# Kernel tuning notes

Measured on AMD Instinct MI355X. Metric: run time of the kernel, lower is better.

Reference implementation:

```python
import jax, jax.numpy as jnp
import numpy as np

N = 262144        # tokens routed
D = 1024          # input_dim
E = 64            # num_experts
TOP_K = 2
NOISE_EPS = 1e-05
ALPHA = 10.0


def setup_inputs() -> dict:
    key = jax.random.key(0)
    k1, k2, k3, k4, k5 = jax.random.split(key, 5)
    x = jax.random.normal(k1, (N, D), dtype=jnp.float32)
    # nn.Linear init scale ~ 1/sqrt(fan_in); keep logits at sane magnitude
    gate_w = jax.random.normal(k2, (E, D), dtype=jnp.float32) * (1.0 / np.sqrt(D))
    gate_b = jax.random.normal(k3, (E,), dtype=jnp.float32) * 0.01
    # w_noise is initialized to zeros in the module; use small random values
    # so the noise path is exercised
    w_noise = jax.random.normal(k4, (E, E), dtype=jnp.float32) * 0.01
    noise = jax.random.normal(k5, (N, E), dtype=jnp.float32)  # torch.randn_like
    return {"x": x, "gate_w": gate_w, "gate_b": gate_b,
            "w_noise": w_noise, "noise": noise}


def reference(x, gate_w, gate_b, w_noise, noise):
    # gate linear: [N, D] @ [D, E] + [E]
    clean_logits = jnp.einsum('nd,ed->ne', x, gate_w) + gate_b
    # training-mode learnable noise injection
    raw_noise_stddev = clean_logits @ w_noise                 # [N, E]
    noise_stddev = jax.nn.softplus(raw_noise_stddev) + NOISE_EPS
    logits = clean_logits + noise * noise_stddev              # noisy_logits

    # decompostion_tp: k-th largest per row (kthvalue(n - k + 1) == k-th largest)
    kth_largest = jax.lax.top_k(logits, TOP_K)[0][:, -1]       # [N]
    mask = logits < kth_largest[:, None]                       # strictly below kth
    sm = jax.nn.softmax(logits, axis=1)
    out = jnp.where(mask,
                    ALPHA * jnp.log1p(sm),      # alpha * log(sm + 1)
                    ALPHA * jnp.expm1(sm))      # alpha * (exp(sm) - 1)

    gates = jax.nn.softmax(out, axis=1)
    return gates
```

## Files before the change

### kernel.cpp

```cpp
#include <hip/hip_runtime.h>

typedef _Float16 half8v __attribute__((ext_vector_type(8)));
typedef float f32x4 __attribute__((ext_vector_type(4)));

constexpr float INV4096 = 1.0f / 4096.0f;
constexpr float ALPHA = 10.0f;

__device__ __forceinline__ f32x4 mfma16(half8v a, half8v b, f32x4 c_) {
  return __builtin_amdgcn_mfma_f32_16x16x32_f16(a, b, c_, 0, 0, 0);
}
__device__ __forceinline__ void dma16(const void *g, void *l) {
  __builtin_amdgcn_global_load_lds(
      (const __attribute__((address_space(1))) void *)g,
      (__attribute__((address_space(3))) void *)l, 16, 0, 0);
}
template <int N> __device__ __forceinline__ void wait_vm() {
  asm volatile("s_waitcnt vmcnt(%0)" ::"n"(N) : "memory");
}

__global__ __launch_bounds__(256) void presplit(const float *__restrict__ GW,
                                                const float *__restrict__ WN,
                                                char *__restrict__ ws) {
  const int b = blockIdx.x;
  const int tid = threadIdx.x;
  if (b < 64) {
    int idx = b * 256 + tid;
    int e = idx >> 8;
    int c4 = idx & 255;
    f32x4 v = *reinterpret_cast<const f32x4 *>(GW + (size_t)idx * 4);
#pragma unroll
    for (int j = 0; j < 4; ++j) {
      int k = c4 * 4 + j;
      float vv = v[j];
      _Float16 hh = (_Float16)vv;
      _Float16 ll = (_Float16)((vv - (float)hh) * 4096.0f);
      int ck = k >> 6, kk = k & 63;
      int off = ck * 16384 + e * 128 + ((((kk >> 3) ^ (e & 7))) << 4) + ((kk & 7) << 1);
      *reinterpret_cast<_Float16 *>(ws + off) = hh;
      *reinterpret_cast<_Float16 *>(ws + off + 8192) = ll;
    }
  } else {
    int idx = (b - 64) * 256 + tid;
    int k = idx >> 4;
    int e0 = (idx & 15) << 2;
    f32x4 v = *reinterpret_cast<const f32x4 *>(WN + (size_t)k * 64 + e0);
#pragma unroll
    for (int j = 0; j < 4; ++j) {
      int e = e0 + j;
      float vv = v[j];
      _Float16 hh = (_Float16)vv;
      _Float16 ll = (_Float16)((vv - (float)hh) * 4096.0f);
      int off = 262144 + e * 128 + ((((k >> 3) ^ (e & 7))) << 4) + ((k & 7) << 1);
      *reinterpret_cast<_Float16 *>(ws + off) = hh;
      *reinterpret_cast<_Float16 *>(ws + off + 8192) = ll;
    }
  }
}

__global__ __launch_bounds__(256, 3) void topk_gating(
    const float *__restrict__ X, const char *__restrict__ WS,
    const float *__restrict__ GB, const float *__restrict__ NZ,
    float *__restrict__ OUT) {
  __shared__ __align__(16) char lds[49152];
  const int tid = threadIdx.x;
  const int lane = tid & 63;
  const int wv = tid >> 6;
  const int q = lane >> 4;
  const int c = lane & 15;
  const int waveRow = blockIdx.x * 64 + wv * 16;

  f32x4 accH[4] = {};
  f32x4 accX[4] = {};
  f32x4 a0[4], a1[4], a2[4];

  const float *xBase = X + (size_t)(waveRow + c) * 1024 + q * 8;
  const char *wsL = WS + wv * 1024 + lane * 16;
  char *ldsL = lds + wv * 1024;

#define LDA4(dst, p)                        \
  {                                         \
    dst[0] = *(const f32x4 *)((p) + 0);     \
    dst[1] = *(const f32x4 *)((p) + 4);     \
    dst[2] = *(const f32x4 *)((p) + 32);    \
    dst[3] = *(const f32x4 *)((p) + 36);    \
  }
#define DMAB(CK)                                                            \
  {                                                                         \
    _Pragma("unroll") for (int i_ = 0; i_ < 4; ++i_)                        \
        dma16(wsL + (CK) * 16384 + i_ * 4096,                               \
              ldsL + ((CK) % 3) * 16384 + i_ * 4096);                       \
  }
#define CONV(A, ah, al)                                           \
  {                                                               \
    _Pragma("unroll") for (int ks_ = 0; ks_ < 2; ++ks_)           \
        _Pragma("unroll") for (int j_ = 0; j_ < 8; ++j_) {        \
      float xv_ = A[ks_ * 2 + (j_ >> 2)][j_ & 3];                 \
      _Float16 hh_ = (_Float16)xv_;                               \
      ah[ks_][j_] = hh_;                                          \
      al[ks_][j_] = (_Float16)((xv_ - (float)hh_) * 4096.0f);     \
    }                                                             \
  }
#define MFMAB(BUF, ah, al)                                                 \
  {                                                                        \
    _Pragma("unroll") for (int ks_ = 0; ks_ < 2; ++ks_)                    \
        _Pragma("unroll") for (int t_ = 0; t_ < 4; ++t_) {                 \
      int e_ = t_ * 16 + c;                                                \
      int off_ = (BUF) + e_ * 128 + ((((ks_ * 4 + q) ^ (e_ & 7))) << 4);   \
      half8v bh_ = *reinterpret_cast<half8v *>(lds + off_);                \
      half8v bl_ = *reinterpret_cast<half8v *>(lds + off_ + 8192);         \
      accH[t_] = mfma16(ah[ks_], bh_, accH[t_]);                           \
      accX[t_] = mfma16(ah[ks_], bl_, accX[t_]);                           \
      accX[t_] = mfma16(al[ks_], bh_, accX[t_]);                           \
    }                                                                      \
  }
#define STEP(KC, ABANK)                                          \
  {                                                              \
    half8v ah[2], al[2];                                         \
    CONV(ABANK, ah, al);                                         \
    if ((KC) + 2 <= 15) DMAB((KC) + 2);                          \
    if ((KC) + 3 <= 15) LDA4(ABANK, xBase + ((KC) + 3) * 64);    \
    MFMAB(((KC) % 3) * 16384, ah, al);                           \
  }
#define BAR() __builtin_amdgcn_s_barrier()

  DMAB(0);
  DMAB(1);
  LDA4(a0, xBase);
  LDA4(a1, xBase + 64);
  LDA4(a2, xBase + 128);
  wait_vm<16>();
  BAR();

  STEP(0, a0)  wait_vm<12>(); BAR();
  STEP(1, a1)  wait_vm<12>(); BAR();
  STEP(2, a2)  wait_vm<12>(); BAR();
  STEP(3, a0)  wait_vm<12>(); BAR();
  STEP(4, a1)  wait_vm<12>(); BAR();
  STEP(5, a2)  wait_vm<12>(); BAR();
  STEP(6, a0)  wait_vm<12>(); BAR();
  STEP(7, a1)  wait_vm<12>(); BAR();
  STEP(8, a2)  wait_vm<12>(); BAR();
  STEP(9, a0)  wait_vm<12>(); BAR();
  STEP(10, a1) wait_vm<12>(); BAR();
  STEP(11, a2) wait_vm<12>(); BAR();
  STEP(12, a0) wait_vm<12>(); BAR();
  STEP(13, a1) wait_vm<8>();  BAR();
  STEP(14, a2) wait_vm<0>();  BAR();
  STEP(15, a0)

  float bs0 = GB[c], bs1 = GB[16 + c], bs2 = GB[32 + c], bs3 = GB[48 + c];
#pragma unroll
  for (int i = 0; i < 4; ++i)
    dma16(wsL + 262144 + i * 4096, ldsL + 16384 + i * 4096);
  asm volatile("" ::: "memory");
  float nz[4][4];
#pragma unroll
  for (int t = 0; t < 4; ++t)
#pragma unroll
    for (int r = 0; r < 4; ++r)
      nz[t][r] = NZ[(size_t)(waveRow + 4 * q + r) * 64 + t * 16 + c];

  float cl[4][4];
  const float bsv[4] = {bs0, bs1, bs2, bs3};
#pragma unroll
  for (int t = 0; t < 4; ++t)
#pragma unroll
    for (int r = 0; r < 4; ++r)
      cl[t][r] = accH[t][r] + accX[t][r] * INV4096 + bsv[t];

  char *cb = lds + 32768 + wv * 4096;
#pragma unroll
  for (int t = 0; t < 4; ++t)
#pragma unroll
    for (int r = 0; r < 4; ++r) {
      int row = 4 * q + r;
      int colf = t * 16 + c;
      int off = row * 256 + ((((colf >> 2) ^ row)) << 4) + ((colf & 3) << 2);
      *reinterpret_cast<float *>(cb + off) = cl[t][r];
    }
  wait_vm<16>();
  BAR();

  f32x4 rH[4] = {};
  f32x4 rX[4] = {};
#pragma unroll
  for (int ks = 0; ks < 2; ++ks) {
    int slot0 = ks * 8 + q * 2;
    f32x4 va = *reinterpret_cast<f32x4 *>(cb + c * 256 + (((slot0 ^ c)) << 4));
    f32x4 vb = *reinterpret_cast<f32x4 *>(cb + c * 256 + ((((slot0 + 1) ^ c)) << 4));
    half8v ah, al;
#pragma unroll
    for (int j = 0; j < 4; ++j) {
      float v = va[j];
      _Float16 hh = (_Float16)v;
      ah[j] = hh;
      al[j] = (_Float16)((v - (float)hh) * 4096.0f);
      float v2 = vb[j];
      _Float16 h2 = (_Float16)v2;
      ah[4 + j] = h2;
      al[4 + j] = (_Float16)((v2 - (float)h2) * 4096.0f);
    }
#pragma unroll
    for (int t = 0; t < 4; ++t) {
      int e = t * 16 + c;
      int off = 16384 + e * 128 + ((((ks * 4 + q) ^ (e & 7))) << 4);
      half8v bh = *reinterpret_cast<half8v *>(lds + off);
      half8v bl = *reinterpret_cast<half8v *>(lds + off + 8192);
      rH[t] = mfma16(ah, bh, rH[t]);
      rX[t] = mfma16(ah, bl, rX[t]);
      rX[t] = mfma16(al, bh, rX[t]);
    }
  }

  float lg[4][4];
#pragma unroll
  for (int t = 0; t < 4; ++t)
#pragma unroll
    for (int r = 0; r < 4; ++r) {
      float raw = rH[t][r] + rX[t][r] * INV4096;
      float sp = fmaxf(raw, 0.0f) + __logf(1.0f + __expf(-fabsf(raw)));
      lg[r][t] = cl[t][r] + nz[t][r] * (sp + 1e-5f);
    }

#pragma unroll
  for (int r = 0; r < 4; ++r) {
    float v0 = lg[r][0], v1 = lg[r][1], v2 = lg[r][2], v3 = lg[r][3];
    float a = fmaxf(v0, v1), b_ = fminf(v0, v1);
    float d1 = fmaxf(v2, v3), d2 = fminf(v2, v3);
    float m1 = fmaxf(a, d1);
    float m2 = fmaxf(fminf(a, d1), fmaxf(b_, d2));
#pragma unroll
    for (int s = 1; s <= 8; s <<= 1) {
      float om1 = __shfl_xor(m1, s, 64);
      float om2 = __shfl_xor(m2, s, 64);
      float hi = fmaxf(m1, om1);
      float lo = fminf(m1, om1);
      float sec = (m1 >= om1) ? m2 : om2;
      m2 = fmaxf(lo, sec);
      m1 = hi;
    }
    float se[4], ssum = 0.f;
#pragma unroll
    for (int t = 0; t < 4; ++t) {
      se[t] = __expf(lg[r][t] - m1);
      ssum += se[t];
    }
#pragma unroll
    for (int s = 1; s <= 8; s <<= 1) ssum += __shfl_xor(ssum, s, 64);
    float inv = 1.0f / ssum;
    float ov[4];
#pragma unroll
    for (int t = 0; t < 4; ++t) {
      float sm = se[t] * inv;
      float vlog = ALPHA * __logf(1.0f + sm);
      float vexp = ALPHA * (__expf(sm) - 1.0f);
      ov[t] = (lg[r][t] < m2) ? vlog : vexp;
    }
    float g = fmaxf(fmaxf(ov[0], ov[1]), fmaxf(ov[2], ov[3]));
#pragma unroll
    for (int s = 1; s <= 8; s <<= 1) g = fmaxf(g, __shfl_xor(g, s, 64));
    float gsum = 0.f;
#pragma unroll
    for (int t = 0; t < 4; ++t) {
      ov[t] = __expf(ov[t] - g);
      gsum += ov[t];
    }
#pragma unroll
    for (int s = 1; s <= 8; s <<= 1) gsum += __shfl_xor(gsum, s, 64);
    float ginv = 1.0f / gsum;
    size_t rowOff = (size_t)(waveRow + 4 * q + r) * 64;
#pragma unroll
    for (int t = 0; t < 4; ++t)
      OUT[rowOff + t * 16 + c] = ov[t] * ginv;
  }
}

extern "C" void kernel_launch(void *const *d_in, const int *in_sizes, int n_in,
                              void *d_out, int out_size, void *d_ws,
                              size_t ws_size, hipStream_t stream) {
  const float *x = (const float *)d_in[0];
  const float *gw = (const float *)d_in[1];
  const float *gb = (const float *)d_in[2];
  const float *wn = (const float *)d_in[3];
  const float *nz = (const float *)d_in[4];
  float *out = (float *)d_out;
  char *ws = (char *)d_ws;
  const int N = in_sizes[0] / 1024;

  hipLaunchKernelGGL(presplit, dim3(68), dim3(256), 0, stream, gw, wn, ws);
  hipLaunchKernelGGL(topk_gating, dim3(N / 64), dim3(256), 0, stream, x, ws,
                     gb, nz, out);
}
```

Before: 274.3 us.

## Replace rolling triple-buffered K pipeline with four batched load-then-compute phases

Replaces the software-pipelined 16-step loop, which prefetched weight chunks two steps ahead into a 3-slot LDS ring and X three steps ahead, with four phases. Each phase loads four K-chunks of weights into a 64KB LDS buffer and four chunks of X into registers, waits for all of them, then computes. LDS grows to 64KB and the occupancy hint drops from 3 to 2 blocks per CU. This cuts barrier and waitcnt count but removes the overlap between memory and MFMA within a block, so hiding latency now relies on other resident blocks.

```diff
diff --git a/kernel.cpp b/kernel.cpp
--- a/kernel.cpp
+++ b/kernel.cpp
@@ -57,11 +57,11 @@
   }
 }
 
-__global__ __launch_bounds__(256, 3) void topk_gating(
+__global__ __launch_bounds__(256, 2) void topk_gating(
     const float *__restrict__ X, const char *__restrict__ WS,
     const float *__restrict__ GB, const float *__restrict__ NZ,
     float *__restrict__ OUT) {
-  __shared__ __align__(16) char lds[49152];
+  __shared__ __align__(16) char lds[65536];
   const int tid = threadIdx.x;
   const int lane = tid & 63;
   const int wv = tid >> 6;
@@ -71,25 +71,12 @@
 
   f32x4 accH[4] = {};
   f32x4 accX[4] = {};
-  f32x4 a0[4], a1[4], a2[4];
+  f32x4 aR[4][4];
 
   const float *xBase = X + (size_t)(waveRow + c) * 1024 + q * 8;
   const char *wsL = WS + wv * 1024 + lane * 16;
   char *ldsL = lds + wv * 1024;
 
-#define LDA4(dst, p)                        \
-  {                                         \
-    dst[0] = *(const f32x4 *)((p) + 0);     \
-    dst[1] = *(const f32x4 *)((p) + 4);     \
-    dst[2] = *(const f32x4 *)((p) + 32);    \
-    dst[3] = *(const f32x4 *)((p) + 36);    \
-  }
-#define DMAB(CK)                                                            \
-  {                                                                         \
-    _Pragma("unroll") for (int i_ = 0; i_ < 4; ++i_)                        \
-        dma16(wsL + (CK) * 16384 + i_ * 4096,                               \
-              ldsL + ((CK) % 3) * 16384 + i_ * 4096);                       \
-  }
 #define CONV(A, ah, al)                                           \
   {                                                               \
     _Pragma("unroll") for (int ks_ = 0; ks_ < 2; ++ks_)           \
@@ -113,45 +100,39 @@
       accX[t_] = mfma16(al[ks_], bh_, accX[t_]);                           \
     }                                                                      \
   }
-#define STEP(KC, ABANK)                                          \
-  {                                                              \
-    half8v ah[2], al[2];                                         \
-    CONV(ABANK, ah, al);                                         \
-    if ((KC) + 2 <= 15) DMAB((KC) + 2);                          \
-    if ((KC) + 3 <= 15) LDA4(ABANK, xBase + ((KC) + 3) * 64);    \
-    MFMAB(((KC) % 3) * 16384, ah, al);                           \
-  }
 #define BAR() __builtin_amdgcn_s_barrier()
 
-  DMAB(0);
-  DMAB(1);
-  LDA4(a0, xBase);
-  LDA4(a1, xBase + 64);
-  LDA4(a2, xBase + 128);
-  wait_vm<16>();
-  BAR();
-
-  STEP(0, a0)  wait_vm<12>(); BAR();
-  STEP(1, a1)  wait_vm<12>(); BAR();
-  STEP(2, a2)  wait_vm<12>(); BAR();
-  STEP(3, a0)  wait_vm<12>(); BAR();
-  STEP(4, a1)  wait_vm<12>(); BAR();
-  STEP(5, a2)  wait_vm<12>(); BAR();
-  STEP(6, a0)  wait_vm<12>(); BAR();
-  STEP(7, a1)  wait_vm<12>(); BAR();
-  STEP(8, a2)  wait_vm<12>(); BAR();
-  STEP(9, a0)  wait_vm<12>(); BAR();
-  STEP(10, a1) wait_vm<12>(); BAR();
-  STEP(11, a2) wait_vm<12>(); BAR();
-  STEP(12, a0) wait_vm<12>(); BAR();
-  STEP(13, a1) wait_vm<8>();  BAR();
-  STEP(14, a2) wait_vm<0>();  BAR();
-  STEP(15, a0)
+#pragma unroll
+  for (int m = 0; m < 4; ++m) {
+#pragma unroll
+    for (int j = 0; j < 4; ++j)
+#pragma unroll
+      for (int i = 0; i < 4; ++i)
+        dma16(wsL + (m * 4 + j) * 16384 + i * 4096,
+              ldsL + j * 16384 + i * 4096);
+#pragma unroll
+    for (int s = 0; s < 4; ++s) {
+      const float *xp = xBase + (m * 4 + s) * 64;
+      aR[s][0] = *(const f32x4 *)(xp + 0);
+      aR[s][1] = *(const f32x4 *)(xp + 4);
+      aR[s][2] = *(const f32x4 *)(xp + 32);
+      aR[s][3] = *(const f32x4 *)(xp + 36);
+    }
+    wait_vm<0>();
+    BAR();
+#pragma unroll
+    for (int s = 0; s < 4; ++s) {
+      half8v ah[2], al[2];
+      CONV(aR[s], ah, al);
+      MFMAB(s * 16384, ah, al);
+    }
+    BAR();
+  }
 
   float bs0 = GB[c], bs1 = GB[16 + c], bs2 = GB[32 + c], bs3 = GB[48 + c];
 #pragma unroll
   for (int i = 0; i < 4; ++i)
-    dma16(wsL + 262144 + i * 4096, ldsL + 16384 + i * 4096);
+    dma16(wsL + 262144 + i * 4096, ldsL + i * 4096);
   asm volatile("" ::: "memory");
   float nz[4][4];
 #pragma unroll
@@ -168,7 +149,7 @@
     for (int r = 0; r < 4; ++r)
       cl[t][r] = accH[t][r] + accX[t][r] * INV4096 + bsv[t];
 
-  char *cb = lds + 32768 + wv * 4096;
+  char *cb = lds + 16384 + wv * 4096;
 #pragma unroll
   for (int t = 0; t < 4; ++t)
 #pragma unroll
@@ -203,7 +184,7 @@
 #pragma unroll
     for (int t = 0; t < 4; ++t) {
       int e = t * 16 + c;
-      int off = 16384 + e * 128 + ((((ks * 4 + q) ^ (e & 7))) << 4);
+      int off = e * 128 + ((((ks * 4 + q) ^ (e & 7))) << 4);
       half8v bh = *reinterpret_cast<half8v *>(lds + off);
       half8v bl = *reinterpret_cast<half8v *>(lds + off + 8192);
       rH[t] = mfma16(ah, bh, rH[t]);
```

New measurement: 296.6 us. 8.1% more time.
